# Optimization experiments

Measured on AMD Instinct MI355X. Metric: run time of the kernel, lower is better.

## Reference

```python
import jax, jax.numpy as jnp
import numpy as np

B, T, D, H = 8, 2048, 512, 128

def setup_inputs() -> dict:
    key = jax.random.key(0)
    ks = jax.random.split(key, 8)
    s = lambda fan_in: 1.0 / np.sqrt(fan_in)
    return {
        "x": jax.random.normal(ks[0], (B, T, D), jnp.float32),
        "prediction": jax.random.normal(ks[1], (B, T, D), jnp.float32),
        "Wq": jax.random.uniform(ks[2], (D, H), jnp.float32, -s(D), s(D)),
        "bq": jnp.zeros((H,), jnp.float32),
        "Wk": jax.random.uniform(ks[3], (D, H), jnp.float32, -s(D), s(D)),
        "bk": jnp.zeros((H,), jnp.float32),
        "Wv": jax.random.uniform(ks[4], (D, D), jnp.float32, -s(D), s(D)),
        "bv": jnp.zeros((D,), jnp.float32),
        "Wf": jax.random.uniform(ks[5], (2 * D, D), jnp.float32, -s(2 * D), s(2 * D)),
        "bf": jnp.zeros((D,), jnp.float32),
    }

def reference(x, prediction, Wq, bq, Wk, bk, Wv, bv, Wf, bf):
    # q,k: [B,T,H]; v: [B,T,D]
    q = jnp.einsum('btd,dh->bth', prediction, Wq) + bq
    k = jnp.einsum('btd,dh->bth', x, Wk) + bk
    v = jnp.einsum('btd,de->bte', x, Wv) + bv
    # unscaled attention scores [B,T,T]
    scores = jnp.einsum('bth,bsh->bts', q, k)
    attn = jax.nn.softmax(scores, axis=-1)
    attended = jnp.einsum('bts,bsd->btd', attn, v)
    fusion_input = jnp.concatenate([prediction, attended], axis=-1)  # [B,T,2D]
    return jax.nn.sigmoid(jnp.einsum('btf,fd->btd', fusion_input, Wf) + bf)
```

## Files before the change

kernel.cpp:

```cpp
#include <hip/hip_runtime.h>
#include <hip/hip_bf16.h>


#define APF_B 8
#define APF_T 2048
#define APF_D 512
#define APF_H 128
#define APF_M (APF_B * APF_T)

typedef unsigned short u16;
typedef __attribute__((ext_vector_type(8))) short short8;
typedef __attribute__((ext_vector_type(4))) float f32x4;

static __device__ __forceinline__ float bf2f(u16 u) {
    union { unsigned int i; float f; } w;
    w.i = ((unsigned int)u) << 16;
    return w.f;
}
static __device__ __forceinline__ u16 f2bf(float x) {
    union { float f; unsigned int u; } cv;
    cv.f = x;
    unsigned int u = cv.u + 0x7FFFu + ((cv.u >> 16) & 1u);
    return (u16)(u >> 16);
}

static __device__ __forceinline__ void load16_lds(const u16* g, u16* l) {
    __builtin_amdgcn_global_load_lds(
        (const __attribute__((address_space(1))) unsigned int*)g,
        (__attribute__((address_space(3))) unsigned int*)l,
        16, 0, 0);
}


__global__ __launch_bounds__(256) void cvt_pair(const float* __restrict__ in0,
                                                u16* __restrict__ out0,
                                                const float* __restrict__ in1,
                                                u16* __restrict__ out1, long n4)
{
    long i = blockIdx.x * 256L + threadIdx.x;
    const long stride = (long)gridDim.x * 256L;
    for (; i < 2 * n4; i += stride) {
        const float* in = (i < n4) ? in0 : in1;
        u16* out = (i < n4) ? out0 : out1;
        const long j = (i < n4) ? i : (i - n4);
        const float4 v = ((const float4*)in)[j];
        ushort4 o;
        o.x = f2bf(v.x); o.y = f2bf(v.y); o.z = f2bf(v.z); o.w = f2bf(v.w);
        ((ushort4*)out)[j] = o;
    }
}

__global__ __launch_bounds__(256) void prep_weights(
    const float* __restrict__ Wq, u16* __restrict__ WqT,
    const float* __restrict__ Wk, u16* __restrict__ WkT,
    const float* __restrict__ Wv, u16* __restrict__ WvT,
    const float* __restrict__ Wf, u16* __restrict__ WfT)
{
    const long e = blockIdx.x * 256L + threadIdx.x;
    if (e < 65536) {
        const long idx = e;
        const long n = idx / 512, k = idx % 512;
        WqT[idx] = f2bf(Wq[k * 128 + n]);
    } else if (e < 131072) {
        const long idx = e - 65536;
        const long n = idx / 512, k = idx % 512;
        WkT[idx] = f2bf(Wk[k * 128 + n]);
    } else if (e < 393216) {
        const long idx = e - 131072;
        const long n = idx / 512, k = idx % 512;
        WvT[idx] = f2bf(Wv[k * 512 + n]);
    } else if (e < 917504) {
        const long idx = e - 393216;
        const long n = idx / 1024, k = idx % 1024;
        WfT[idx] = f2bf(Wf[k * 512 + n]);
    }
}

template <int DUAL, int EPI, int BIASM>
__global__ __launch_bounds__(256) void mfma_gemm(
    const u16* __restrict__ Ap, const u16* __restrict__ A2p, long lda,
    const u16* __restrict__ Bp, const u16* __restrict__ Bp2, long ldb,
    const float* __restrict__ biasp, const float* __restrict__ bias2,
    void* __restrict__ Cp, void* __restrict__ Cp2, long ldc, int K,
    long sA, long sB, long sC)
{
    __shared__ u16 smA[128 * 32];
    __shared__ u16 smB[128 * 32];

    const int tid  = threadIdx.x;
    const int lane = tid & 63;
    const int wid  = tid >> 6;
    const int wr   = wid >> 1;
    const int wc   = wid & 1;

    const long row0 = (long)blockIdx.y * 128;
    const long col0 = (long)blockIdx.x * 128;
    const long z    = blockIdx.z;

    const u16* Abase = (DUAL == 2) ? (z ? A2p : Ap) : (Ap + z * sA);
    const u16* Bbase = (DUAL == 2) ? (z ? Bp2 : Bp) : (Bp + z * sB);

    f32x4 acc[4][4];
#pragma unroll
    for (int i = 0; i < 4; ++i)
#pragma unroll
        for (int j = 0; j < 4; ++j)
            acc[i][j] = (f32x4){0.f, 0.f, 0.f, 0.f};

    const int lrow = (lane >> 4) * 4;
    const int lcol = lane & 15;
    const int q8   = (lane >> 4) * 8;

    for (int kb = 0; kb < K; kb += 32) {
#pragma unroll
        for (int rep = 0; rep < 2; ++rep) {
            const int c  = tid + rep * 256;
            const int r  = c >> 2;
            const int kc = (c & 3) * 8;
            const int wbase = (wid * 64 + rep * 256) * 8;
            const u16* ga;
            if (DUAL == 1 && (kb + kc) >= APF_D) {
                ga = A2p + (row0 + r) * lda + (kb + kc - APF_D);
            } else {
                ga = Abase + (row0 + r) * lda + (kb + kc);
            }
            load16_lds(ga, &smA[wbase]);
            const u16* gb = Bbase + (col0 + r) * ldb + (kb + kc);
            load16_lds(gb, &smB[wbase]);
        }
        __syncthreads();

        short8 av[4], bv4[4];
#pragma unroll
        for (int ti = 0; ti < 4; ++ti)
            av[ti] = *(const short8*)&smA[(wr * 64 + ti * 16 + lcol) * 32 + q8];
#pragma unroll
        for (int tj = 0; tj < 4; ++tj)
            bv4[tj] = *(const short8*)&smB[(wc * 64 + tj * 16 + lcol) * 32 + q8];

#pragma unroll
        for (int ti = 0; ti < 4; ++ti)
#pragma unroll
            for (int tj = 0; tj < 4; ++tj)
                acc[ti][tj] = __builtin_amdgcn_mfma_f32_16x16x32_bf16(
                    av[ti], bv4[tj], acc[ti][tj], 0, 0, 0);
        __syncthreads();
    }

    const float* bias = (DUAL == 2 && z) ? bias2 : biasp;

#pragma unroll
    for (int ti = 0; ti < 4; ++ti) {
        const long m0t = row0 + wr * 64 + ti * 16 + lrow;
#pragma unroll
        for (int tj = 0; tj < 4; ++tj) {
            const long n = col0 + wc * 64 + tj * 16 + lcol;
            const float bn = (BIASM == 0 && bias != nullptr) ? bias[n] : 0.f;
            if (EPI == 0) {
                u16* C = (u16*)((DUAL == 2 && z) ? Cp2 : Cp) + ((DUAL == 2) ? 0 : z * sC);
#pragma unroll
                for (int r = 0; r < 4; ++r) {
                    const float bm = (BIASM == 1) ? bias[m0t + r] : bn;
                    C[(m0t + r) * ldc + n] = f2bf(acc[ti][tj][r] + bm);
                }
            } else {
                float* C = (float*)Cp;
#pragma unroll
                for (int r = 0; r < 4; ++r) {
                    const float val = acc[ti][tj][r] + bn;
                    C[(m0t + r) * ldc + n] = 1.0f / (1.0f + expf(-val));
                }
            }
        }
    }
}

#define FA_LDQ 136
#define FA_LDK 136
#define FA_LDV 72
#define FA_LDP 72

__global__ __launch_bounds__(256, 2) void attn_fused(
    const u16* __restrict__ qg, const u16* __restrict__ kg,
    const u16* __restrict__ vTg, u16* __restrict__ attg)
{
    __shared__ u16 sQ[64 * FA_LDQ];
    __shared__ u16 sK[64 * FA_LDK];
    __shared__ u16 sV[256 * FA_LDV];
    __shared__ u16 sP[64 * FA_LDP];

    const int tid  = threadIdx.x;
    const int lane = tid & 63;
    const int w    = tid >> 6;
    const int l15  = lane & 15;
    const int q4   = lane >> 4;

    const long z  = blockIdx.z;
    const long q0 = (long)blockIdx.y * 64;
    const long d0 = (long)blockIdx.x * 256;

    {
        const u16* src = qg + (z * APF_T + q0) * APF_H;
#pragma unroll
        for (int rep = 0; rep < 4; ++rep) {
            const int c   = tid + rep * 256;
            const int row = c >> 4;
            const int c8  = (c & 15) * 8;
            *(uint4*)&sQ[row * FA_LDQ + c8] = *(const uint4*)(src + (long)c * 8);
        }
    }

    f32x4 oacc[16];
#pragma unroll
    for (int i = 0; i < 16; ++i) oacc[i] = (f32x4){0.f, 0.f, 0.f, 0.f};
    float rs[4] = {0.f, 0.f, 0.f, 0.f};

    for (int kt = 0; kt < APF_T / 64; ++kt) {
        __syncthreads();
        {
            const u16* src = kg + (z * APF_T + (long)kt * 64) * APF_H;
#pragma unroll
            for (int rep = 0; rep < 4; ++rep) {
                const int c   = tid + rep * 256;
                const int row = c >> 4;
                const int c8  = (c & 15) * 8;
                *(uint4*)&sK[row * FA_LDK + c8] = *(const uint4*)(src + (long)c * 8);
            }
        }
        {
            const u16* src = vTg + z * ((long)APF_D * APF_T) + d0 * APF_T + (long)kt * 64;
#pragma unroll
            for (int rep = 0; rep < 8; ++rep) {
                const int c   = tid + rep * 256;
                const int row = c >> 3;
                const int c8  = (c & 7) * 8;
                *(uint4*)&sV[row * FA_LDV + c8] =
                    *(const uint4*)(src + (long)row * APF_T + c8);
            }
        }
        __syncthreads();

        f32x4 sacc[4];
#pragma unroll
        for (int tj = 0; tj < 4; ++tj) sacc[tj] = (f32x4){0.f, 0.f, 0.f, 0.f};
#pragma unroll
        for (int kk = 0; kk < 4; ++kk) {
            const short8 av = *(const short8*)&sQ[(w * 16 + l15) * FA_LDQ + kk * 32 + q4 * 8];
#pragma unroll
            for (int tj = 0; tj < 4; ++tj) {
                const short8 bv = *(const short8*)&sK[(tj * 16 + l15) * FA_LDK + kk * 32 + q4 * 8];
                sacc[tj] = __builtin_amdgcn_mfma_f32_16x16x32_bf16(av, bv, sacc[tj], 0, 0, 0);
            }
        }
#pragma unroll
        for (int tj = 0; tj < 4; ++tj)
#pragma unroll
            for (int r = 0; r < 4; ++r) {
                const float e = __expf(sacc[tj][r]);
                rs[r] += e;
                sP[(w * 16 + q4 * 4 + r) * FA_LDP + tj * 16 + l15] = f2bf(e);
            }
#pragma unroll
        for (int kk = 0; kk < 2; ++kk) {
            const short8 ap = *(const short8*)&sP[(w * 16 + l15) * FA_LDP + kk * 32 + q4 * 8];
#pragma unroll
            for (int dt = 0; dt < 16; ++dt) {
                const short8 bv = *(const short8*)&sV[(dt * 16 + l15) * FA_LDV + kk * 32 + q4 * 8];
                oacc[dt] = __builtin_amdgcn_mfma_f32_16x16x32_bf16(ap, bv, oacc[dt], 0, 0, 0);
            }
        }
    }

#pragma unroll
    for (int r = 0; r < 4; ++r) {
        float s = rs[r];
        s += __shfl_xor(s, 1);
        s += __shfl_xor(s, 2);
        s += __shfl_xor(s, 4);
        s += __shfl_xor(s, 8);
        rs[r] = 1.0f / s;
    }

    const long mbase = z * APF_T + q0 + w * 16 + q4 * 4;
#pragma unroll
    for (int dt = 0; dt < 16; ++dt) {
        const long col = d0 + dt * 16 + l15;
#pragma unroll
        for (int r = 0; r < 4; ++r)
            attg[(mbase + r) * APF_D + col] = f2bf(oacc[dt][r] * rs[r]);
    }
}

extern "C" void kernel_launch(void* const* d_in, const int* in_sizes, int n_in,
                              void* d_out, int out_size, void* d_ws, size_t ws_size,
                              hipStream_t stream)
{
    (void)in_sizes; (void)n_in; (void)out_size; (void)ws_size;

    const float* x    = (const float*)d_in[0];
    const float* pred = (const float*)d_in[1];
    const float* Wq   = (const float*)d_in[2];
    const float* bq   = (const float*)d_in[3];
    const float* Wk   = (const float*)d_in[4];
    const float* bk   = (const float*)d_in[5];
    const float* Wv   = (const float*)d_in[6];
    const float* bv   = (const float*)d_in[7];
    const float* Wf   = (const float*)d_in[8];
    const float* bfu  = (const float*)d_in[9];

    u16* wsp   = (u16*)d_ws;
    u16* xb    = wsp;
    u16* predb = xb    + (long)APF_M * APF_D;
    u16* qb    = predb + (long)APF_M * APF_D;
    u16* kbuf  = qb    + (long)APF_M * APF_H;
    u16* vTb   = kbuf  + (long)APF_M * APF_H;
    u16* attb  = vTb   + (long)APF_M * APF_D;
    u16* WqT   = attb  + (long)APF_M * APF_D;
    u16* WkT   = WqT   + (long)APF_H * APF_D;
    u16* WvT   = WkT   + (long)APF_H * APF_D;
    u16* WfT   = WvT   + (long)APF_D * APF_D;

    const dim3 thr(256);
    const long nBTD4 = (long)APF_M * APF_D / 4;

    cvt_pair<<<dim3(1024), thr, 0, stream>>>(x, xb, pred, predb, nBTD4);
    prep_weights<<<dim3(3584), thr, 0, stream>>>(Wq, WqT, Wk, WkT, Wv, WvT, Wf, WfT);

    mfma_gemm<2, 0, 0><<<dim3(1, 128, 2), thr, 0, stream>>>(
        predb, xb, APF_D, WqT, WkT, APF_D, bq, bk, qb, kbuf, APF_H, APF_D,
        0, 0, 0);

    mfma_gemm<0, 0, 1><<<dim3(16, 4, 8), thr, 0, stream>>>(
        WvT, nullptr, APF_D, xb, nullptr, APF_D, bv, nullptr, vTb, nullptr,
        APF_T, APF_D, 0, (long)APF_T * APF_D, (long)APF_D * APF_T);

    attn_fused<<<dim3(2, 32, 8), thr, 0, stream>>>(qb, kbuf, vTb, attb);

    mfma_gemm<1, 2, 0><<<dim3(4, 128, 1), thr, 0, stream>>>(
        predb, attb, APF_D, WfT, nullptr, 2 * APF_D, bfu, nullptr, d_out, nullptr,
        APF_D, 2 * APF_D, 0, 0, 0);
}
```

Measured before the change: 288.6 us.

## Repartition PV matmul so each wave owns a 64-column slice of all query rows

The P·V stage in the fused attention kernel changes its work split. Each wave used to compute its own 16 query rows across all 256 output columns, reading every V tile from LDS. Now each wave computes all 64 query rows for a 64-column slice, so V fragments are loaded once and reused across four row tiles, while P fragments are read from every wave's rows. The change adds a block barrier after writing P and shares row normalizers through LDS before the final store.

```diff
diff --git a/kernel.cpp b/kernel.cpp
--- a/kernel.cpp
+++ b/kernel.cpp
@@ -188,6 +188,7 @@
     __shared__ u16 sK[64 * FA_LDK];
     __shared__ u16 sV[256 * FA_LDV];
     __shared__ u16 sP[64 * FA_LDP];
+    __shared__ float sRS[64];
 
     const int tid  = threadIdx.x;
     const int lane = tid & 63;
@@ -210,9 +211,12 @@
         }
     }
 
-    f32x4 oacc[16];
-#pragma unroll
-    for (int i = 0; i < 16; ++i) oacc[i] = (f32x4){0.f, 0.f, 0.f, 0.f};
+    f32x4 oacc[4][4];
+#pragma unroll
+    for (int i = 0; i < 4; ++i)
+#pragma unroll
+        for (int j = 0; j < 4; ++j)
+            oacc[i][j] = (f32x4){0.f, 0.f, 0.f, 0.f};
     float rs[4] = {0.f, 0.f, 0.f, 0.f};
 
     for (int kt = 0; kt < APF_T / 64; ++kt) {
@@ -260,13 +264,21 @@
                 rs[r] += e;
                 sP[(w * 16 + q4 * 4 + r) * FA_LDP + tj * 16 + l15] = f2bf(e);
             }
+        __syncthreads();
+
 #pragma unroll
         for (int kk = 0; kk < 2; ++kk) {
-            const short8 ap = *(const short8*)&sP[(w * 16 + l15) * FA_LDP + kk * 32 + q4 * 8];
-#pragma unroll
-            for (int dt = 0; dt < 16; ++dt) {
-                const short8 bv = *(const short8*)&sV[(dt * 16 + l15) * FA_LDV + kk * 32 + q4 * 8];
-                oacc[dt] = __builtin_amdgcn_mfma_f32_16x16x32_bf16(ap, bv, oacc[dt], 0, 0, 0);
+            short8 ap[4];
+#pragma unroll
+            for (int ti = 0; ti < 4; ++ti)
+                ap[ti] = *(const short8*)&sP[(ti * 16 + l15) * FA_LDP + kk * 32 + q4 * 8];
+#pragma unroll
+            for (int dt = 0; dt < 4; ++dt) {
+                const short8 bv = *(const short8*)&sV[(w * 64 + dt * 16 + l15) * FA_LDV + kk * 32 + q4 * 8];
+#pragma unroll
+                for (int ti = 0; ti < 4; ++ti)
+                    oacc[ti][dt] = __builtin_amdgcn_mfma_f32_16x16x32_bf16(
+                        ap[ti], bv, oacc[ti][dt], 0, 0, 0);
             }
         }
     }
@@ -280,14 +292,28 @@
         s += __shfl_xor(s, 8);
         rs[r] = 1.0f / s;
     }
-
-    const long mbase = z * APF_T + q0 + w * 16 + q4 * 4;
-#pragma unroll
-    for (int dt = 0; dt < 16; ++dt) {
-        const long col = d0 + dt * 16 + l15;
+    if (l15 == 0) {
 #pragma unroll
         for (int r = 0; r < 4; ++r)
-            attg[(mbase + r) * APF_D + col] = f2bf(oacc[dt][r] * rs[r]);
+            sRS[w * 16 + q4 * 4 + r] = rs[r];
+    }
+    __syncthreads();
+
+    const long rowbase = z * APF_T + q0;
+#pragma unroll
+    for (int ti = 0; ti < 4; ++ti) {
+        float inv[4];
+#pragma unroll
+        for (int r = 0; r < 4; ++r)
+            inv[r] = sRS[ti * 16 + q4 * 4 + r];
+#pragma unroll
+        for (int dt = 0; dt < 4; ++dt) {
+            const long col = d0 + w * 64 + dt * 16 + l15;
+#pragma unroll
+            for (int r = 0; r < 4; ++r)
+                attg[(rowbase + ti * 16 + q4 * 4 + r) * APF_D + col] =
+                    f2bf(oacc[ti][dt][r] * inv[r]);
+        }
     }
 }
 
```

Result: no change. 286.2 us (-0.8%).

## Restructure attention kernel with 32x32 MFMA, XOR-swizzled LDS, register-prefetched K

Applied to the files above, without the earlier changes.

Rewrites the fused attention kernel to use 32x32x16 MFMA tiles with 128-key blocks. Each wave now owns a 32-key slice for QK^T and a 64-column slice of the output for PV. V is read straight from global into registers instead of being staged in LDS. K for the next block is prefetched into registers, LDS padding is replaced by XOR swizzling, and row sums are reduced across waves through LDS. Blocks are remapped to a 1D grid with the batch index in the low bits. The aim is fewer LDS round trips and syncs per key and better MFMA efficiency, at the cost of more register pressure, an extra barrier per block and uncached global V loads.

```diff
diff --git a/kernel.cpp b/kernel.cpp
--- a/kernel.cpp
+++ b/kernel.cpp
@@ -7,16 +7,13 @@
 #define APF_D 512
 #define APF_H 128
 #define APF_M (APF_B * APF_T)
+#define FA_SB 128
 
 typedef unsigned short u16;
 typedef __attribute__((ext_vector_type(8))) short short8;
 typedef __attribute__((ext_vector_type(4))) float f32x4;
-
-static __device__ __forceinline__ float bf2f(u16 u) {
-    union { unsigned int i; float f; } w;
-    w.i = ((unsigned int)u) << 16;
-    return w.f;
-}
+typedef __attribute__((ext_vector_type(16))) float f32x16;
+
 static __device__ __forceinline__ u16 f2bf(float x) {
     union { float f; unsigned int u; } cv;
     cv.f = x;
@@ -29,6 +26,13 @@
         (const __attribute__((address_space(1))) unsigned int*)g,
         (__attribute__((address_space(3))) unsigned int*)l,
         16, 0, 0);
+}
+
+static __device__ __forceinline__ f32x16 zero16() {
+    f32x16 v;
+#pragma unroll
+    for (int i = 0; i < 16; ++i) v[i] = 0.f;
+    return v;
 }
 
 
@@ -175,120 +179,195 @@
     }
 }
 
-#define FA_LDQ 136
-#define FA_LDK 136
-#define FA_LDV 72
-#define FA_LDP 72
-
 __global__ __launch_bounds__(256, 2) void attn_fused(
     const u16* __restrict__ qg, const u16* __restrict__ kg,
     const u16* __restrict__ vTg, u16* __restrict__ attg)
 {
-    __shared__ u16 sQ[64 * FA_LDQ];
-    __shared__ u16 sK[64 * FA_LDK];
-    __shared__ u16 sV[256 * FA_LDV];
-    __shared__ u16 sP[64 * FA_LDP];
+    __shared__ u16 sQ[64 * 128];
+    __shared__ u16 sK[128 * 128];
+    __shared__ u16 sP[64 * 128];
+    __shared__ float sRSp[256];
 
     const int tid  = threadIdx.x;
     const int lane = tid & 63;
     const int w    = tid >> 6;
-    const int l15  = lane & 15;
-    const int q4   = lane >> 4;
-
-    const long z  = blockIdx.z;
-    const long q0 = (long)blockIdx.y * 64;
-    const long d0 = (long)blockIdx.x * 256;
+    const int l31  = lane & 31;
+    const int hi   = lane >> 5;
+
+    const int  bid = blockIdx.x;
+    const long z   = bid & 7;
+    const int  r   = bid >> 3;
+    const long q0  = (long)(r & 31) * 64;
+    const long d0  = (long)(r >> 5) * 256;
 
     {
         const u16* src = qg + (z * APF_T + q0) * APF_H;
 #pragma unroll
         for (int rep = 0; rep < 4; ++rep) {
-            const int c   = tid + rep * 256;
-            const int row = c >> 4;
-            const int c8  = (c & 15) * 8;
-            *(uint4*)&sQ[row * FA_LDQ + c8] = *(const uint4*)(src + (long)c * 8);
-        }
-    }
-
-    f32x4 oacc[16];
-#pragma unroll
-    for (int i = 0; i < 16; ++i) oacc[i] = (f32x4){0.f, 0.f, 0.f, 0.f};
-    float rs[4] = {0.f, 0.f, 0.f, 0.f};
-
-    for (int kt = 0; kt < APF_T / 64; ++kt) {
+            const int c    = tid + rep * 256;
+            const int row  = c >> 4;
+            const int col8 = (c & 15) * 8;
+            *(uint4*)&sQ[row * 128 + (col8 ^ ((row & 7) << 3))] =
+                *(const uint4*)(src + (long)c * 8);
+        }
+    }
+
+    f32x16 oacc[2][2];
+#pragma unroll
+    for (int i = 0; i < 2; ++i)
+#pragma unroll
+        for (int j = 0; j < 2; ++j) oacc[i][j] = zero16();
+    f32x16 rsacc[2];
+    rsacc[0] = zero16(); rsacc[1] = zero16();
+
+    const u16* kbase0 = kg + z * (long)APF_T * APF_H;
+    const u16* vzbase = vTg + z * ((long)APF_D * APF_T) + (d0 + (long)w * 64) * APF_T;
+
+    uint4 kst[8];
+#pragma unroll
+    for (int rep = 0; rep < 8; ++rep) {
+        const int c = tid + rep * 256;
+        kst[rep] = *(const uint4*)(kbase0 + (long)c * 8);
+    }
+
+    for (int kt = 0; kt < APF_T / FA_SB; ++kt) {
         __syncthreads();
+#pragma unroll
+        for (int rep = 0; rep < 8; ++rep) {
+            const int c    = tid + rep * 256;
+            const int row  = c >> 4;
+            const int col8 = (c & 15) * 8;
+            *(uint4*)&sK[row * 128 + (col8 ^ ((row & 7) << 3))] = kst[rep];
+        }
+        __syncthreads();
+
+        f32x16 sacc[2];
+        sacc[0] = zero16(); sacc[1] = zero16();
+#pragma unroll
+        for (int ks = 0; ks < 8; ++ks) {
+            const int colk = ks * 16 + hi * 8;
+            const int krow = w * 32 + l31;
+            const short8 bv = *(const short8*)&sK[krow * 128 + (colk ^ ((krow & 7) << 3))];
+#pragma unroll
+            for (int qt = 0; qt < 2; ++qt) {
+                const int qrow = qt * 32 + l31;
+                const short8 av = *(const short8*)&sQ[qrow * 128 + (colk ^ ((qrow & 7) << 3))];
+                sacc[qt] = __builtin_amdgcn_mfma_f32_32x32x16_bf16(av, bv, sacc[qt], 0, 0, 0);
+            }
+        }
+
+        const u16* vkt = vzbase + (long)kt * FA_SB;
+        short8 vf1[2][4];
+#pragma unroll
+        for (int dt = 0; dt < 2; ++dt)
+#pragma unroll
+            for (int ks = 0; ks < 4; ++ks)
+                vf1[dt][ks] = *(const short8*)(vkt + (long)(dt * 32 + l31) * APF_T + ks * 16 + hi * 8);
+
+#pragma unroll
+        for (int qt = 0; qt < 2; ++qt)
+#pragma unroll
+            for (int rg = 0; rg < 16; ++rg) {
+                const float e = __expf(sacc[qt][rg]);
+                rsacc[qt][rg] += e;
+                const int prow = qt * 32 + (rg & 3) + 8 * (rg >> 2) + 4 * hi;
+                const int pcol = w * 32 + l31;
+                sP[prow * 128 + (pcol ^ ((prow & 7) << 3))] = f2bf(e);
+            }
+        __syncthreads();
+
+#pragma unroll
+        for (int ks = 0; ks < 4; ++ks) {
+            const int colk = ks * 16 + hi * 8;
+            short8 pa[2];
+#pragma unroll
+            for (int qt = 0; qt < 2; ++qt) {
+                const int prow = qt * 32 + l31;
+                pa[qt] = *(const short8*)&sP[prow * 128 + (colk ^ ((prow & 7) << 3))];
+            }
+#pragma unroll
+            for (int dt = 0; dt < 2; ++dt)
+#pragma unroll
+                for (int qt = 0; qt < 2; ++qt)
+                    oacc[qt][dt] = __builtin_amdgcn_mfma_f32_32x32x16_bf16(
+                        pa[qt], vf1[dt][ks], oacc[qt][dt], 0, 0, 0);
+        }
+
+        short8 vf2[2][4];
+#pragma unroll
+        for (int dt = 0; dt < 2; ++dt)
+#pragma unroll
+            for (int ks = 0; ks < 4; ++ks)
+                vf2[dt][ks] = *(const short8*)(vkt + (long)(dt * 32 + l31) * APF_T + (ks + 4) * 16 + hi * 8);
         {
-            const u16* src = kg + (z * APF_T + (long)kt * 64) * APF_H;
-#pragma unroll
-            for (int rep = 0; rep < 4; ++rep) {
-                const int c   = tid + rep * 256;
-                const int row = c >> 4;
-                const int c8  = (c & 15) * 8;
-                *(uint4*)&sK[row * FA_LDK + c8] = *(const uint4*)(src + (long)c * 8);
-            }
-        }
-        {
-            const u16* src = vTg + z * ((long)APF_D * APF_T) + d0 * APF_T + (long)kt * 64;
+            const int ktn = (kt + 1 < APF_T / FA_SB) ? kt + 1 : kt;
+            const u16* ksrc = kbase0 + (long)ktn * FA_SB * APF_H;
 #pragma unroll
             for (int rep = 0; rep < 8; ++rep) {
-                const int c   = tid + rep * 256;
-                const int row = c >> 3;
-                const int c8  = (c & 7) * 8;
-                *(uint4*)&sV[row * FA_LDV + c8] =
-                    *(const uint4*)(src + (long)row * APF_T + c8);
-            }
-        }
-        __syncthreads();
-
-        f32x4 sacc[4];
-#pragma unroll
-        for (int tj = 0; tj < 4; ++tj) sacc[tj] = (f32x4){0.f, 0.f, 0.f, 0.f};
-#pragma unroll
-        for (int kk = 0; kk < 4; ++kk) {
-            const short8 av = *(const short8*)&sQ[(w * 16 + l15) * FA_LDQ + kk * 32 + q4 * 8];
-#pragma unroll
-            for (int tj = 0; tj < 4; ++tj) {
-                const short8 bv = *(const short8*)&sK[(tj * 16 + l15) * FA_LDK + kk * 32 + q4 * 8];
-                sacc[tj] = __builtin_amdgcn_mfma_f32_16x16x32_bf16(av, bv, sacc[tj], 0, 0, 0);
-            }
-        }
-#pragma unroll
-        for (int tj = 0; tj < 4; ++tj)
-#pragma unroll
-            for (int r = 0; r < 4; ++r) {
-                const float e = __expf(sacc[tj][r]);
-                rs[r] += e;
-                sP[(w * 16 + q4 * 4 + r) * FA_LDP + tj * 16 + l15] = f2bf(e);
-            }
-#pragma unroll
-        for (int kk = 0; kk < 2; ++kk) {
-            const short8 ap = *(const short8*)&sP[(w * 16 + l15) * FA_LDP + kk * 32 + q4 * 8];
-#pragma unroll
-            for (int dt = 0; dt < 16; ++dt) {
-                const short8 bv = *(const short8*)&sV[(dt * 16 + l15) * FA_LDV + kk * 32 + q4 * 8];
-                oacc[dt] = __builtin_amdgcn_mfma_f32_16x16x32_bf16(ap, bv, oacc[dt], 0, 0, 0);
-            }
-        }
-    }
-
-#pragma unroll
-    for (int r = 0; r < 4; ++r) {
-        float s = rs[r];
-        s += __shfl_xor(s, 1);
-        s += __shfl_xor(s, 2);
-        s += __shfl_xor(s, 4);
-        s += __shfl_xor(s, 8);
-        rs[r] = 1.0f / s;
-    }
-
-    const long mbase = z * APF_T + q0 + w * 16 + q4 * 4;
-#pragma unroll
-    for (int dt = 0; dt < 16; ++dt) {
-        const long col = d0 + dt * 16 + l15;
-#pragma unroll
-        for (int r = 0; r < 4; ++r)
-            attg[(mbase + r) * APF_D + col] = f2bf(oacc[dt][r] * rs[r]);
-    }
+                const int c = tid + rep * 256;
+                kst[rep] = *(const uint4*)(ksrc + (long)c * 8);
+            }
+        }
+
+#pragma unroll
+        for (int ks = 0; ks < 4; ++ks) {
+            const int colk = (ks + 4) * 16 + hi * 8;
+            short8 pa[2];
+#pragma unroll
+            for (int qt = 0; qt < 2; ++qt) {
+                const int prow = qt * 32 + l31;
+                pa[qt] = *(const short8*)&sP[prow * 128 + (colk ^ ((prow & 7) << 3))];
+            }
+#pragma unroll
+            for (int dt = 0; dt < 2; ++dt)
+#pragma unroll
+                for (int qt = 0; qt < 2; ++qt)
+                    oacc[qt][dt] = __builtin_amdgcn_mfma_f32_32x32x16_bf16(
+                        pa[qt], vf2[dt][ks], oacc[qt][dt], 0, 0, 0);
+        }
+    }
+
+#pragma unroll
+    for (int qt = 0; qt < 2; ++qt)
+#pragma unroll
+        for (int rg = 0; rg < 16; ++rg) {
+            float s = rsacc[qt][rg];
+            s += __shfl_xor(s, 1);
+            s += __shfl_xor(s, 2);
+            s += __shfl_xor(s, 4);
+            s += __shfl_xor(s, 8);
+            s += __shfl_xor(s, 16);
+            rsacc[qt][rg] = s;
+        }
+    if (l31 == 0) {
+#pragma unroll
+        for (int qt = 0; qt < 2; ++qt)
+#pragma unroll
+            for (int rg = 0; rg < 16; ++rg) {
+                const int row = qt * 32 + (rg & 3) + 8 * (rg >> 2) + 4 * hi;
+                sRSp[w * 64 + row] = rsacc[qt][rg];
+            }
+    }
+    __syncthreads();
+    if (tid < 64) {
+        const float t = sRSp[tid] + sRSp[64 + tid] + sRSp[128 + tid] + sRSp[192 + tid];
+        sRSp[tid] = 1.0f / t;
+    }
+    __syncthreads();
+
+    const long rowg0 = z * APF_T + q0;
+    const long colg0 = d0 + (long)w * 64;
+#pragma unroll
+    for (int qt = 0; qt < 2; ++qt)
+#pragma unroll
+        for (int rg = 0; rg < 16; ++rg) {
+            const int row = qt * 32 + (rg & 3) + 8 * (rg >> 2) + 4 * hi;
+            const float inv = sRSp[row];
+#pragma unroll
+            for (int dt = 0; dt < 2; ++dt)
+                attg[(rowg0 + row) * APF_D + colg0 + dt * 32 + l31] =
+                    f2bf(oacc[qt][dt][rg] * inv);
+        }
 }
 
 extern "C" void kernel_launch(void* const* d_in, const int* in_sizes, int n_in,
@@ -334,7 +413,7 @@
         WvT, nullptr, APF_D, xb, nullptr, APF_D, bv, nullptr, vTb, nullptr,
         APF_T, APF_D, 0, (long)APF_T * APF_D, (long)APF_D * APF_T);
 
-    attn_fused<<<dim3(2, 32, 8), thr, 0, stream>>>(qb, kbuf, vTb, attb);
+    attn_fused<<<dim3(512), thr, 0, stream>>>(qb, kbuf, vTb, attb);
 
     mfma_gemm<1, 2, 0><<<dim3(4, 128, 1), thr, 0, stream>>>(
         predb, attb, APF_D, WfT, nullptr, 2 * APF_D, bfu, nullptr, d_out, nullptr,
```

After: 353.4 us. +22.5%, slower.
